# Kernel optimization log

Hardware: AMD Instinct MI355X
Metric: run time of the kernel (lower is better)

Reference implementation:

```python
import jax, jax.numpy as jnp
import numpy as np

B, M, H = 8, 2048, 1024


def setup_inputs() -> dict:
    key = jax.random.key(0)
    k0, k1, k2, k3, k4 = jax.random.split(key, 5)
    return {
        "query": jax.random.normal(k0, (B, M, H), dtype=jnp.float32),
        "key": jax.random.normal(k1, (B, M, H), dtype=jnp.float32),
        "span": jax.random.uniform(k2, (B, M, 2), dtype=jnp.float32),
        "value": jax.random.normal(k3, (B, M, H), dtype=jnp.float32),
        "key_pe": jax.random.normal(k4, (1, H, M), dtype=jnp.float32),
    }


def reference(query, key, span, value, key_pe):
    # Faithful to the source's returned value:
    #   attn_cont (span-gathered version) is overwritten by the dense q @ k^T,
    #   and the scaled/softmaxed `attn` (content + positional) is computed but
    #   NEVER used for the output. The module returns attn_cont @ value with
    #   no scaling and no softmax. span / key_pe do not affect the output.
    attn_cont = jnp.einsum('bmh,bnh->bmn', query, key)  # [B, M, M]
    out = jnp.matmul(attn_cont, value)                   # [B, M, H]
    return out
```

## Files before the change

kernel.cpp:

```cpp
#include <hip/hip_runtime.h>
#include <hip/hip_bf16.h>

typedef __attribute__((ext_vector_type(4))) float f32x4;
typedef __attribute__((ext_vector_type(8))) short bf16x8;
typedef unsigned short u16;


__device__ __forceinline__ u16 f2bf(float f) {
  union { float f; unsigned int u; } v;
  v.f = f;
  unsigned int r = (v.u + 0x7fffu + ((v.u >> 16) & 1u)) >> 16;
  return (u16)r;
}

__device__ __forceinline__ void async16(const void* g, const void* l) {
  __builtin_amdgcn_global_load_lds(
      (const __attribute__((address_space(1))) unsigned int*)(unsigned long)g,
      (__attribute__((address_space(3))) unsigned int*)(unsigned int)(unsigned long)l,
      16, 0, 0);
}


__global__ __launch_bounds__(256) void cvt_plain(const float* __restrict__ in,
                                                 u16* __restrict__ out, int n4) {
  int stride = gridDim.x * blockDim.x;
  for (int i = blockIdx.x * blockDim.x + threadIdx.x; i < n4; i += stride) {
    f32x4 v = *(const f32x4*)(in + (long)i * 4);
    ushort4 o;
    o.x = f2bf(v.x); o.y = f2bf(v.y); o.z = f2bf(v.z); o.w = f2bf(v.w);
    *(ushort4*)(out + (long)i * 4) = o;
  }
}


__global__ __launch_bounds__(256) void cvt_transpose(const float* __restrict__ in,
                                                     u16* __restrict__ out,
                                                     int R, int C) {
  __shared__ u16 tile[64][68];
  const long bo = (long)blockIdx.z * (long)R * (long)C;
  const int r0 = blockIdx.y * 64;
  const int c0 = blockIdx.x * 64;
  const int t = threadIdx.x;
  const int tr = t >> 4;
  const int tc4 = (t & 15) * 4;

#pragma unroll
  for (int i = 0; i < 4; ++i) {
    int r = i * 16 + tr;
    f32x4 v = *(const f32x4*)(in + bo + (long)(r0 + r) * C + c0 + tc4);
    tile[tc4 + 0][r] = f2bf(v.x);
    tile[tc4 + 1][r] = f2bf(v.y);
    tile[tc4 + 2][r] = f2bf(v.z);
    tile[tc4 + 3][r] = f2bf(v.w);
  }
  __syncthreads();
#pragma unroll
  for (int i = 0; i < 4; ++i) {
    int c = i * 16 + tr;
    ushort4 u = *(const ushort4*)(&tile[c][tc4]);
    *(ushort4*)(out + bo + (long)(c0 + c) * R + r0 + tc4) = u;
  }
}


#define BM 128
#define BN 128
#define BK 32

template <bool BF16OUT>
__global__ __launch_bounds__(256, 3) void gemm_nt(const u16* __restrict__ A,
                                                  const u16* __restrict__ Bt,
                                                  void* __restrict__ Cv,
                                                  int M, int N, int K,
                                                  long sA, long sB, long sC) {
  __shared__ u16 As[2][BM][BK];
  __shared__ u16 Bs[2][BN][BK];

  const int b = blockIdx.z;
  A  += (long)b * sA;
  Bt += (long)b * sB;

  const int bn0 = blockIdx.x * BN;
  const int bm0 = blockIdx.y * BM;

  const int tid  = threadIdx.x;
  const int lane = tid & 63;
  const int wave = tid >> 6;
  const int wr = wave >> 1;
  const int wc = wave & 1;
  const int l16 = lane & 15;
  const int kh  = lane >> 4;

  const u16* Abase = A + (long)bm0 * K;
  const u16* Bbase = Bt + (long)bn0 * K;

  const int u0 = wave * 64 + lane;

  f32x4 acc[4][4] = {};

  const int NT = K / BK;
  int cur = 0;

#pragma unroll
  for (int i = 0; i < 2; ++i) {
    int u = i * 256 + u0;
    async16(Abase + (long)(u >> 2) * K + (u & 3) * 8,
            (const char*)(&As[0][0][0]) + i * 4096 + wave * 1024);
    async16(Bbase + (long)(u >> 2) * K + (u & 3) * 8,
            (const char*)(&Bs[0][0][0]) + i * 4096 + wave * 1024);
  }
  asm volatile("s_waitcnt vmcnt(0)" ::: "memory");
  __syncthreads();

  for (int t = 0; t < NT; ++t) {
    if (t + 1 < NT) {
      const int k0 = (t + 1) * BK;
      const int nb = cur ^ 1;
#pragma unroll
      for (int i = 0; i < 2; ++i) {
        int u = i * 256 + u0;
        async16(Abase + k0 + (long)(u >> 2) * K + (u & 3) * 8,
                (const char*)(&As[nb][0][0]) + i * 4096 + wave * 1024);
        async16(Bbase + k0 + (long)(u >> 2) * K + (u & 3) * 8,
                (const char*)(&Bs[nb][0][0]) + i * 4096 + wave * 1024);
      }
    }

    bf16x8 af[4], bfr[4];
#pragma unroll
    for (int i = 0; i < 4; ++i) {
      af[i]  = *(const bf16x8*)(&As[cur][wr * 64 + i * 16 + l16][kh * 8]);
      bfr[i] = *(const bf16x8*)(&Bs[cur][wc * 64 + i * 16 + l16][kh * 8]);
    }
#pragma unroll
    for (int i = 0; i < 4; ++i)
#pragma unroll
      for (int j = 0; j < 4; ++j)
        acc[i][j] =
            __builtin_amdgcn_mfma_f32_16x16x32_bf16(af[i], bfr[j], acc[i][j], 0, 0, 0);

    asm volatile("s_waitcnt vmcnt(0)" ::: "memory");
    __syncthreads();
    cur ^= 1;
  }

  u16*   Cb = (u16*)Cv + (long)b * sC;
  float* Cf = (float*)Cv + (long)b * sC;
#pragma unroll
  for (int i = 0; i < 4; ++i) {
    const int gm = bm0 + wr * 64 + i * 16 + kh * 4;
#pragma unroll
    for (int j = 0; j < 4; ++j) {
      const int gn = bn0 + wc * 64 + j * 16 + l16;
#pragma unroll
      for (int r = 0; r < 4; ++r) {
        if (BF16OUT)
          Cb[(long)(gm + r) * N + gn] = f2bf(acc[i][j][r]);
        else
          Cf[(long)(gm + r) * N + gn] = acc[i][j][r];
      }
    }
  }
}


extern "C" void kernel_launch(void* const* d_in, const int* in_sizes, int n_in,
                              void* d_out, int out_size, void* d_ws, size_t ws_size,
                              hipStream_t stream) {
  const float* Q  = (const float*)d_in[0];
  const float* Kf = (const float*)d_in[1];
  const float* V  = (const float*)d_in[3];
  float* out = (float*)d_out;

  const int B = 8, M = 2048, H = 1024;
  const size_t bmh2 = (size_t)B * M * H * 2;

  char* ws = (char*)d_ws;
  u16* Qb = (u16*)(ws);
  u16* Kt = (u16*)(ws + bmh2);
  u16* Vt = (u16*)(ws + 2 * bmh2);
  u16* Pt = (u16*)(ws + 3 * bmh2);

  cvt_plain<<<2048, 256, 0, stream>>>(Q, Qb, B * M * H / 4);
  cvt_transpose<<<dim3(H / 64, M / 64, B), 256, 0, stream>>>(Kf, Kt, M, H);
  cvt_transpose<<<dim3(H / 64, M / 64, B), 256, 0, stream>>>(V, Vt, M, H);

  gemm_nt<true><<<dim3(H / BN, H / BM, B), 256, 0, stream>>>(
      Vt, Kt, (void*)Pt, H, H, M, (long)H * M, (long)H * M, (long)H * H);

  gemm_nt<false><<<dim3(H / BN, M / BM, B), 256, 0, stream>>>(
      Qb, Pt, (void*)out, M, H, H, (long)M * H, (long)H * H, (long)M * H);
}
```

Baseline: 162.0 us.

## Fuse fp32-to-bf16 conversion and transpose into larger-tile pipelined GEMMs

Removes the three separate conversion/transpose kernels and loads fp32 inputs directly inside the GEMMs, packing to bf16 with v_cvt_pk_bf16_f32 and writing transposed into XOR-swizzled LDS. GEMM tiles grow to 128x256 and 256x256 with 512-thread blocks and a BK of 64. Register prefetch of the next tile is interleaved with MFMA halves under s_setprio, and batch-interleaved block ordering is used. This cuts the extra global round trips for the bf16 copies and the launch overhead, at the cost of higher register pressure and more complex LDS layouts.

```diff
diff --git a/kernel.cpp b/kernel.cpp
--- a/kernel.cpp
+++ b/kernel.cpp
@@ -3,7 +3,9 @@
 
 typedef __attribute__((ext_vector_type(4))) float f32x4;
 typedef __attribute__((ext_vector_type(8))) short bf16x8;
+typedef __attribute__((ext_vector_type(2))) unsigned int u32x2;
 typedef unsigned short u16;
+typedef unsigned int u32;
 
 
 __device__ __forceinline__ u16 f2bf(float f) {
@@ -13,6 +15,12 @@
   return (u16)r;
 }
 
+__device__ __forceinline__ u32 pk2(float a, float b) {
+  u32 r;
+  asm("v_cvt_pk_bf16_f32 %0, %1, %2" : "=v"(r) : "v"(a), "v"(b));
+  return r;
+}
+
 __device__ __forceinline__ void async16(const void* g, const void* l) {
   __builtin_amdgcn_global_load_lds(
       (const __attribute__((address_space(1))) unsigned int*)(unsigned long)g,
@@ -20,147 +28,373 @@
       16, 0, 0);
 }
 
-
-__global__ __launch_bounds__(256) void cvt_plain(const float* __restrict__ in,
-                                                 u16* __restrict__ out, int n4) {
-  int stride = gridDim.x * blockDim.x;
-  for (int i = blockIdx.x * blockDim.x + threadIdx.x; i < n4; i += stride) {
-    f32x4 v = *(const f32x4*)(in + (long)i * 4);
-    ushort4 o;
-    o.x = f2bf(v.x); o.y = f2bf(v.y); o.z = f2bf(v.z); o.w = f2bf(v.w);
-    *(ushort4*)(out + (long)i * 4) = o;
-  }
-}
-
-
-__global__ __launch_bounds__(256) void cvt_transpose(const float* __restrict__ in,
-                                                     u16* __restrict__ out,
-                                                     int R, int C) {
-  __shared__ u16 tile[64][68];
-  const long bo = (long)blockIdx.z * (long)R * (long)C;
-  const int r0 = blockIdx.y * 64;
-  const int c0 = blockIdx.x * 64;
-  const int t = threadIdx.x;
-  const int tr = t >> 4;
-  const int tc4 = (t & 15) * 4;
-
-#pragma unroll
-  for (int i = 0; i < 4; ++i) {
-    int r = i * 16 + tr;
-    f32x4 v = *(const f32x4*)(in + bo + (long)(r0 + r) * C + c0 + tc4);
-    tile[tc4 + 0][r] = f2bf(v.x);
-    tile[tc4 + 1][r] = f2bf(v.y);
-    tile[tc4 + 2][r] = f2bf(v.z);
-    tile[tc4 + 3][r] = f2bf(v.w);
-  }
-  __syncthreads();
-#pragma unroll
-  for (int i = 0; i < 4; ++i) {
-    int c = i * 16 + tr;
-    ushort4 u = *(const ushort4*)(&tile[c][tc4]);
-    *(ushort4*)(out + bo + (long)(c0 + c) * R + r0 + tc4) = u;
-  }
-}
-
-
-#define BM 128
-#define BN 128
-#define BK 32
-
-template <bool BF16OUT>
-__global__ __launch_bounds__(256, 3) void gemm_nt(const u16* __restrict__ A,
-                                                  const u16* __restrict__ Bt,
-                                                  void* __restrict__ Cv,
-                                                  int M, int N, int K,
-                                                  long sA, long sB, long sC) {
-  __shared__ u16 As[2][BM][BK];
-  __shared__ u16 Bs[2][BN][BK];
-
-  const int b = blockIdx.z;
-  A  += (long)b * sA;
-  Bt += (long)b * sB;
-
-  const int bn0 = blockIdx.x * BN;
-  const int bm0 = blockIdx.y * BM;
-
-  const int tid  = threadIdx.x;
+__device__ __forceinline__ void bar() {
+  asm volatile("" ::: "memory");
+  __builtin_amdgcn_s_barrier();
+  asm volatile("" ::: "memory");
+}
+
+#define WAIT_LGKM0() asm volatile("s_waitcnt lgkmcnt(0)" ::: "memory")
+#define WAIT_VM0()   asm volatile("s_waitcnt vmcnt(0)" ::: "memory")
+
+#define G8(r) ((((r) >> 3) ^ (r)) & 7)
+
+__global__ __launch_bounds__(512, 2) void gemmA(const float* __restrict__ V,
+                                                const float* __restrict__ Kf,
+                                                u16* __restrict__ Pt) {
+  __shared__ u16 As[2][128][64];
+  __shared__ u16 Bs[2][256][64];
+
+  const int bid = blockIdx.x;
+  const int b = bid & 7;
+  const int tile = bid >> 3;
+  const int bn0 = (tile & 3) * 256;
+  const int bm0 = (tile >> 2) * 128;
+
+  const int tid = threadIdx.x;
   const int lane = tid & 63;
   const int wave = tid >> 6;
-  const int wr = wave >> 1;
-  const int wc = wave & 1;
+  const int wr = wave >> 2;
+  const int wc = wave & 3;
   const int l16 = lane & 15;
-  const int kh  = lane >> 4;
-
-  const u16* Abase = A + (long)bm0 * K;
-  const u16* Bbase = Bt + (long)bn0 * K;
-
-  const int u0 = wave * 64 + lane;
+  const int kh = lane >> 4;
+
+  const int dq = tid & 31, nq = tid >> 5;
+
+  const char* pV = (const char*)(V + (long)b * 2048 * 1024 +
+                                 (long)(nq * 4) * 1024 + bm0 + dq * 4);
+  const char* pK = (const char*)(Kf + (long)b * 2048 * 1024 +
+                                 (long)(nq * 4) * 1024 + bn0 + dq * 4);
+
+  int awo[4], bwo[2][4];
+#pragma unroll
+  for (int j = 0; j < 4; ++j) {
+    int r = dq * 4 + j;
+    awo[j] = r * 128 + (((nq >> 1) ^ G8(r)) * 16) + (nq & 1) * 8;
+  }
+#pragma unroll
+  for (int h = 0; h < 2; ++h)
+#pragma unroll
+    for (int j = 0; j < 4; ++j) {
+      int r = h * 128 + dq * 4 + j;
+      bwo[h][j] = r * 128 + (((nq >> 1) ^ G8(r)) * 16) + (nq & 1) * 8;
+    }
+
+  int offA[2][2][2], offB[2][2][2];
+#pragma unroll
+  for (int q = 0; q < 2; ++q)
+#pragma unroll
+    for (int f = 0; f < 2; ++f) {
+      int rA = q * 64 + wr * 32 + f * 16 + l16;
+      int rB = q * 128 + wc * 32 + f * 16 + l16;
+#pragma unroll
+      for (int ks = 0; ks < 2; ++ks) {
+        offA[q][f][ks] = rA * 64 + (((ks * 4 + kh) ^ G8(rA)) * 8);
+        offB[q][f][ks] = rB * 64 + (((ks * 4 + kh) ^ G8(rB)) * 8);
+      }
+    }
 
   f32x4 acc[4][4] = {};
-
-  const int NT = K / BK;
-  int cur = 0;
-
-#pragma unroll
-  for (int i = 0; i < 2; ++i) {
-    int u = i * 256 + u0;
-    async16(Abase + (long)(u >> 2) * K + (u & 3) * 8,
-            (const char*)(&As[0][0][0]) + i * 4096 + wave * 1024);
-    async16(Bbase + (long)(u >> 2) * K + (u & 3) * 8,
-            (const char*)(&Bs[0][0][0]) + i * 4096 + wave * 1024);
-  }
-  asm volatile("s_waitcnt vmcnt(0)" ::: "memory");
-  __syncthreads();
-
+  f32x4 aq[4], bq[8];
+  bf16x8 ar[2][2], br[4][2];
+
+#pragma unroll
+  for (int j = 0; j < 4; ++j) aq[j] = *(const f32x4*)(pV + j * 4096);
+#pragma unroll
+  for (int h = 0; h < 2; ++h)
+#pragma unroll
+    for (int j = 0; j < 4; ++j)
+      bq[h * 4 + j] = *(const f32x4*)(pK + h * 512 + j * 4096);
+  pV += 262144; pK += 262144;
+  {
+    char* dA = (char*)&As[0][0][0];
+    char* dB = (char*)&Bs[0][0][0];
+#pragma unroll
+    for (int j = 0; j < 4; ++j) {
+      u32x2 v; v.x = pk2(aq[0][j], aq[1][j]); v.y = pk2(aq[2][j], aq[3][j]);
+      *(u32x2*)(dA + awo[j]) = v;
+    }
+#pragma unroll
+    for (int h = 0; h < 2; ++h)
+#pragma unroll
+      for (int j = 0; j < 4; ++j) {
+        u32x2 v; v.x = pk2(bq[h * 4 + 0][j], bq[h * 4 + 1][j]);
+        v.y = pk2(bq[h * 4 + 2][j], bq[h * 4 + 3][j]);
+        *(u32x2*)(dB + bwo[h][j]) = v;
+      }
+  }
+  WAIT_LGKM0();
+  bar();
+
+  const int NT = 32;
   for (int t = 0; t < NT; ++t) {
-    if (t + 1 < NT) {
-      const int k0 = (t + 1) * BK;
-      const int nb = cur ^ 1;
-#pragma unroll
-      for (int i = 0; i < 2; ++i) {
-        int u = i * 256 + u0;
-        async16(Abase + k0 + (long)(u >> 2) * K + (u & 3) * 8,
-                (const char*)(&As[nb][0][0]) + i * 4096 + wave * 1024);
-        async16(Bbase + k0 + (long)(u >> 2) * K + (u & 3) * 8,
-                (const char*)(&Bs[nb][0][0]) + i * 4096 + wave * 1024);
+    const int cur = t & 1, nxt = cur ^ 1;
+    const bool g = (t + 1 < NT);
+    const u16* Ab = &As[cur][0][0];
+    const u16* Bb = &Bs[cur][0][0];
+
+#pragma unroll
+    for (int f = 0; f < 2; ++f)
+#pragma unroll
+      for (int ks = 0; ks < 2; ++ks)
+        ar[f][ks] = *(const bf16x8*)(Ab + offA[0][f][ks]);
+#pragma unroll
+    for (int q = 0; q < 2; ++q)
+#pragma unroll
+      for (int f = 0; f < 2; ++f)
+#pragma unroll
+        for (int ks = 0; ks < 2; ++ks)
+          br[q * 2 + f][ks] = *(const bf16x8*)(Bb + offB[q][f][ks]);
+
+    if (g) {
+#pragma unroll
+      for (int j = 0; j < 4; ++j) aq[j] = *(const f32x4*)(pV + j * 4096);
+#pragma unroll
+      for (int h = 0; h < 2; ++h)
+#pragma unroll
+        for (int j = 0; j < 4; ++j)
+          bq[h * 4 + j] = *(const f32x4*)(pK + h * 512 + j * 4096);
+      pV += 262144; pK += 262144;
+    }
+
+    __builtin_amdgcn_s_setprio(1);
+#pragma unroll
+    for (int f = 0; f < 2; ++f)
+#pragma unroll
+      for (int n = 0; n < 4; ++n)
+#pragma unroll
+        for (int ks = 0; ks < 2; ++ks)
+          acc[f][n] = __builtin_amdgcn_mfma_f32_16x16x32_bf16(
+              ar[f][ks], br[n][ks], acc[f][n], 0, 0, 0);
+    __builtin_amdgcn_s_setprio(0);
+
+#pragma unroll
+    for (int f = 0; f < 2; ++f)
+#pragma unroll
+      for (int ks = 0; ks < 2; ++ks)
+        ar[f][ks] = *(const bf16x8*)(Ab + offA[1][f][ks]);
+
+    if (g) {
+      char* dA = (char*)&As[nxt][0][0];
+      char* dB = (char*)&Bs[nxt][0][0];
+#pragma unroll
+      for (int j = 0; j < 4; ++j) {
+        u32x2 v; v.x = pk2(aq[0][j], aq[1][j]); v.y = pk2(aq[2][j], aq[3][j]);
+        *(u32x2*)(dA + awo[j]) = v;
       }
-    }
-
-    bf16x8 af[4], bfr[4];
-#pragma unroll
-    for (int i = 0; i < 4; ++i) {
-      af[i]  = *(const bf16x8*)(&As[cur][wr * 64 + i * 16 + l16][kh * 8]);
-      bfr[i] = *(const bf16x8*)(&Bs[cur][wc * 64 + i * 16 + l16][kh * 8]);
-    }
-#pragma unroll
-    for (int i = 0; i < 4; ++i)
-#pragma unroll
-      for (int j = 0; j < 4; ++j)
-        acc[i][j] =
-            __builtin_amdgcn_mfma_f32_16x16x32_bf16(af[i], bfr[j], acc[i][j], 0, 0, 0);
-
-    asm volatile("s_waitcnt vmcnt(0)" ::: "memory");
-    __syncthreads();
-    cur ^= 1;
-  }
-
-  u16*   Cb = (u16*)Cv + (long)b * sC;
-  float* Cf = (float*)Cv + (long)b * sC;
-#pragma unroll
-  for (int i = 0; i < 4; ++i) {
-    const int gm = bm0 + wr * 64 + i * 16 + kh * 4;
-#pragma unroll
-    for (int j = 0; j < 4; ++j) {
-      const int gn = bn0 + wc * 64 + j * 16 + l16;
-#pragma unroll
-      for (int r = 0; r < 4; ++r) {
-        if (BF16OUT)
-          Cb[(long)(gm + r) * N + gn] = f2bf(acc[i][j][r]);
-        else
-          Cf[(long)(gm + r) * N + gn] = acc[i][j][r];
+#pragma unroll
+      for (int h = 0; h < 2; ++h)
+#pragma unroll
+        for (int j = 0; j < 4; ++j) {
+          u32x2 v; v.x = pk2(bq[h * 4 + 0][j], bq[h * 4 + 1][j]);
+          v.y = pk2(bq[h * 4 + 2][j], bq[h * 4 + 3][j]);
+          *(u32x2*)(dB + bwo[h][j]) = v;
+        }
+    }
+
+    __builtin_amdgcn_s_setprio(1);
+#pragma unroll
+    for (int f = 0; f < 2; ++f)
+#pragma unroll
+      for (int n = 0; n < 4; ++n)
+#pragma unroll
+        for (int ks = 0; ks < 2; ++ks)
+          acc[2 + f][n] = __builtin_amdgcn_mfma_f32_16x16x32_bf16(
+              ar[f][ks], br[n][ks], acc[2 + f][n], 0, 0, 0);
+    __builtin_amdgcn_s_setprio(0);
+
+    WAIT_LGKM0();
+    bar();
+  }
+
+  u16* Cb = Pt + (long)b * 1024 * 1024;
+#pragma unroll
+  for (int fm = 0; fm < 4; ++fm) {
+    const int gm = bm0 + (fm >> 1) * 64 + wr * 32 + (fm & 1) * 16 + kh * 4;
+#pragma unroll
+    for (int fn = 0; fn < 4; ++fn) {
+      const int gn = bn0 + (fn >> 1) * 128 + wc * 32 + (fn & 1) * 16 + l16;
+#pragma unroll
+      for (int r = 0; r < 4; ++r)
+        Cb[(long)(gm + r) * 1024 + gn] = f2bf(acc[fm][fn][r]);
+    }
+  }
+}
+
+__global__ __launch_bounds__(512, 2) void gemmB(const float* __restrict__ Q,
+                                                const u16* __restrict__ Pt,
+                                                float* __restrict__ out) {
+  __shared__ u16 As[2][256][64];
+  __shared__ u16 Bs[2][2][128][64];
+
+  const int bid = blockIdx.x;
+  const int b = bid & 7;
+  const int tile = bid >> 3;
+  const int bn0 = (tile & 3) * 256;
+  const int bm0 = (tile >> 2) * 256;
+
+  const int tid = threadIdx.x;
+  const int lane = tid & 63;
+  const int wave = tid >> 6;
+  const int wr = wave >> 2;
+  const int wc = wave & 3;
+  const int l16 = lane & 15;
+  const int kh = lane >> 4;
+
+  const int mrow = tid >> 4;
+  const char* pQ = (const char*)(Q + (long)b * 2048 * 1024 +
+                                 (long)(bm0 + mrow) * 1024 + (tid & 15) * 4);
+
+  int qwo[8];
+#pragma unroll
+  for (int p = 0; p < 8; ++p) {
+    int r = p * 32 + mrow;
+    qwo[p] = r * 128 + ((((tid & 15) >> 1) ^ G8(r)) * 16) + (tid & 1) * 8;
+  }
+
+  int boff[2][2];
+#pragma unroll
+  for (int h = 0; h < 2; ++h)
+#pragma unroll
+    for (int i = 0; i < 2; ++i) {
+      int u = tid + i * 512;
+      int row = u >> 3, sl = (u & 7) ^ (row & 7);
+      boff[h][i] = (bn0 + h * 128 + row) * 2048 + sl * 16;
+    }
+  const char* PtB = (const char*)(Pt + (long)b * 1024 * 1024);
+
+  int offA[2][4][2];
+#pragma unroll
+  for (int q = 0; q < 2; ++q)
+#pragma unroll
+    for (int f = 0; f < 4; ++f) {
+      int r = q * 128 + wr * 64 + f * 16 + l16;
+#pragma unroll
+      for (int ks = 0; ks < 2; ++ks)
+        offA[q][f][ks] = r * 64 + (((ks * 4 + kh) ^ G8(r)) * 8);
+    }
+  int offBf[2][2];
+#pragma unroll
+  for (int g_ = 0; g_ < 2; ++g_) {
+    int r = wc * 32 + g_ * 16 + l16;
+#pragma unroll
+    for (int ks = 0; ks < 2; ++ks)
+      offBf[g_][ks] = r * 64 + (((ks * 4 + kh) ^ (l16 & 7)) * 8);
+  }
+
+#define STG_PT(h, buf)                                                      \
+  {                                                                         \
+    _Pragma("unroll") for (int i_ = 0; i_ < 2; ++i_) {                      \
+      async16(PtB + boff[h][i_],                                            \
+              (char*)&Bs[buf][h][0][0] + (tid + i_ * 512) * 16);            \
+      boff[h][i_] += 128;                                                   \
+    }                                                                       \
+  }
+
+  f32x4 acc[8][4] = {};
+  f32x4 qv[8];
+  bf16x8 ar[4][2], br[4][2];
+
+#pragma unroll
+  for (int p = 0; p < 8; ++p) qv[p] = *(const f32x4*)(pQ + p * 131072);
+  STG_PT(0, 0);
+  STG_PT(1, 0);
+  {
+    char* dA = (char*)&As[0][0][0];
+#pragma unroll
+    for (int p = 0; p < 8; ++p) {
+      u32x2 v; v.x = pk2(qv[p].x, qv[p].y); v.y = pk2(qv[p].z, qv[p].w);
+      *(u32x2*)(dA + qwo[p]) = v;
+    }
+  }
+  pQ += 256;
+  WAIT_VM0();
+  WAIT_LGKM0();
+  bar();
+
+  const int NT = 16;
+  for (int t = 0; t < NT; ++t) {
+    const int cur = t & 1, nxt = cur ^ 1;
+    const bool g = (t + 1 < NT);
+    const u16* Ab = &As[cur][0][0];
+
+#pragma unroll
+    for (int f = 0; f < 4; ++f)
+#pragma unroll
+      for (int ks = 0; ks < 2; ++ks)
+        ar[f][ks] = *(const bf16x8*)(Ab + offA[0][f][ks]);
+#pragma unroll
+    for (int qn = 0; qn < 2; ++qn)
+#pragma unroll
+      for (int g_ = 0; g_ < 2; ++g_)
+#pragma unroll
+        for (int ks = 0; ks < 2; ++ks)
+          br[qn * 2 + g_][ks] =
+              *(const bf16x8*)(&Bs[cur][qn][0][0] + offBf[g_][ks]);
+
+    if (g) {
+#pragma unroll
+      for (int p = 0; p < 8; ++p) qv[p] = *(const f32x4*)(pQ + p * 131072);
+      STG_PT(0, nxt);
+      STG_PT(1, nxt);
+    }
+
+    __builtin_amdgcn_s_setprio(1);
+#pragma unroll
+    for (int f = 0; f < 4; ++f)
+#pragma unroll
+      for (int n = 0; n < 4; ++n)
+#pragma unroll
+        for (int ks = 0; ks < 2; ++ks)
+          acc[f][n] = __builtin_amdgcn_mfma_f32_16x16x32_bf16(
+              ar[f][ks], br[n][ks], acc[f][n], 0, 0, 0);
+    __builtin_amdgcn_s_setprio(0);
+
+#pragma unroll
+    for (int f = 0; f < 4; ++f)
+#pragma unroll
+      for (int ks = 0; ks < 2; ++ks)
+        ar[f][ks] = *(const bf16x8*)(Ab + offA[1][f][ks]);
+
+    if (g) {
+      char* dA = (char*)&As[nxt][0][0];
+#pragma unroll
+      for (int p = 0; p < 8; ++p) {
+        u32x2 v; v.x = pk2(qv[p].x, qv[p].y); v.y = pk2(qv[p].z, qv[p].w);
+        *(u32x2*)(dA + qwo[p]) = v;
       }
-    }
-  }
+      pQ += 256;
+    }
+
+    __builtin_amdgcn_s_setprio(1);
+#pragma unroll
+    for (int f = 0; f < 4; ++f)
+#pragma unroll
+      for (int n = 0; n < 4; ++n)
+#pragma unroll
+        for (int ks = 0; ks < 2; ++ks)
+          acc[4 + f][n] = __builtin_amdgcn_mfma_f32_16x16x32_bf16(
+              ar[f][ks], br[n][ks], acc[4 + f][n], 0, 0, 0);
+    __builtin_amdgcn_s_setprio(0);
+
+    if (g) WAIT_VM0();
+    WAIT_LGKM0();
+    bar();
+  }
+
+  float* Cf = out + (long)b * 2048 * 1024;
+#pragma unroll
+  for (int fm = 0; fm < 8; ++fm) {
+    const int gm = bm0 + (fm >> 2) * 128 + wr * 64 + (fm & 3) * 16 + kh * 4;
+#pragma unroll
+    for (int fn = 0; fn < 4; ++fn) {
+      const int gn = bn0 + (fn >> 1) * 128 + wc * 32 + (fn & 1) * 16 + l16;
+#pragma unroll
+      for (int r = 0; r < 4; ++r)
+        Cf[(long)(gm + r) * 1024 + gn] = acc[fm][fn][r];
+    }
+  }
+#undef STG_PT
 }
 
 
@@ -172,22 +406,9 @@
   const float* V  = (const float*)d_in[3];
   float* out = (float*)d_out;
 
-  const int B = 8, M = 2048, H = 1024;
-  const size_t bmh2 = (size_t)B * M * H * 2;
-
-  char* ws = (char*)d_ws;
-  u16* Qb = (u16*)(ws);
-  u16* Kt = (u16*)(ws + bmh2);
-  u16* Vt = (u16*)(ws + 2 * bmh2);
-  u16* Pt = (u16*)(ws + 3 * bmh2);
-
-  cvt_plain<<<2048, 256, 0, stream>>>(Q, Qb, B * M * H / 4);
-  cvt_transpose<<<dim3(H / 64, M / 64, B), 256, 0, stream>>>(Kf, Kt, M, H);
-  cvt_transpose<<<dim3(H / 64, M / 64, B), 256, 0, stream>>>(V, Vt, M, H);
-
-  gemm_nt<true><<<dim3(H / BN, H / BM, B), 256, 0, stream>>>(
-      Vt, Kt, (void*)Pt, H, H, M, (long)H * M, (long)H * M, (long)H * H);
-
-  gemm_nt<false><<<dim3(H / BN, M / BM, B), 256, 0, stream>>>(
-      Qb, Pt, (void*)out, M, H, H, (long)M * H, (long)H * H, (long)M * H);
-}
+  u16* Pt = (u16*)d_ws;
+
+  gemmA<<<256, 512, 0, stream>>>(V, Kf, Pt);
+
+  gemmB<<<256, 512, 0, stream>>>(Q, Pt, out);
+}
```

Measured after the change: 130.8 us. 1.24x faster.
